# Performance work log

Hardware: AMD Instinct MI355X
Metric: run time of the kernel (lower is better)

## Reference

```python
import jax, jax.numpy as jnp
import numpy as np

B, L, C = 2, 2048, 2048
H, HKV, D = 16, 4, 128  # heads, kv heads, head_dim
G = H // HKV            # GQA group size
NEG = -1e9


def rms_norm(x, w, eps=1e-6):
    # FastRMSNorm: compute in fp32, scale by weight, cast back
    xf = x.astype(jnp.float32)
    y = xf * jax.lax.rsqrt(jnp.mean(xf * xf, axis=-1, keepdims=True) + eps) * w
    return y.astype(x.dtype)


def apply_rope(t, cos, sin):
    # t: (B, h, L, D); cos/sin: (L, D//2) broadcast to (1,1,L,D//2)
    t1, t2 = jnp.split(t, 2, axis=-1)
    c = cos[None, None]
    s = sin[None, None]
    return jnp.concatenate([t1 * c - t2 * s, t2 * c + t1 * s], axis=-1)


def setup_inputs() -> dict:
    key = jax.random.key(0)
    ks = jax.random.split(key, 8)
    x = jax.random.normal(ks[0], (B, L, C), jnp.float32)
    Wq = jax.random.normal(ks[1], (H * D, C), jnp.float32) * 0.02
    Wk = jax.random.normal(ks[2], (HKV * D, C), jnp.float32) * 0.02
    Wv = jax.random.normal(ks[3], (HKV * D, C), jnp.float32) * 0.02
    Wo = jax.random.normal(ks[4], (C, H * D), jnp.float32) * 0.02
    q_norm_w = jnp.ones((D,), jnp.float32)
    k_norm_w = jnp.ones((D,), jnp.float32)
    pos = jnp.arange(L, dtype=jnp.float32)[:, None]
    inv_freq = 1.0 / (10000.0 ** (jnp.arange(0, D, 2, dtype=jnp.float32) / D))
    ang = pos * inv_freq[None, :]            # (L, D//2)
    rope_cos = jnp.cos(ang)
    rope_sin = jnp.sin(ang)
    # VAR-style block-causal visibility: 8 blocks of 256, query block i sees key blocks <= i
    blk = jnp.arange(L) // 256
    vis = blk[None, :] <= blk[:, None]       # (L, L) bool
    attn_bias = jnp.where(vis, 0.0, NEG).astype(jnp.float32)[None, None]  # (1,1,L,L)
    return dict(x=x, Wq=Wq, Wk=Wk, Wv=Wv, Wo=Wo, q_norm_w=q_norm_w,
                k_norm_w=k_norm_w, rope_cos=rope_cos, rope_sin=rope_sin,
                attn_bias=attn_bias)


def reference(x, Wq, Wk, Wv, Wo, q_norm_w, k_norm_w, rope_cos, rope_sin, attn_bias):
    b, l, c = x.shape
    # fused projections -> (B, h, L, D)
    q = rms_norm((x @ Wq.T).reshape(b, l, H, D), q_norm_w).transpose(0, 2, 1, 3)
    k = rms_norm((x @ Wk.T).reshape(b, l, HKV, D), k_norm_w).transpose(0, 2, 1, 3)
    v = (x @ Wv.T).reshape(b, l, HKV, D).transpose(0, 2, 1, 3)
    q = apply_rope(q, rope_cos, rope_sin)
    k = apply_rope(k, rope_cos, rope_sin)
    scale = D ** -0.5
    # GQA: group query heads over kv heads
    qg = q.reshape(b, HKV, G, l, D)
    scores = jnp.einsum('bkgqd,bkKd->bkgqK', qg, k) * scale
    scores = scores + attn_bias[:, :, None]  # broadcast (1,1,1,L,L)
    probs = jax.nn.softmax(scores, axis=-1)
    out = jnp.einsum('bkgqK,bkKd->bkgqd', probs, v)
    out = out.reshape(b, H, l, D).transpose(0, 2, 1, 3).reshape(b, l, H * D)
    return out @ Wo.T
```

## Files before the change

### kernel.cpp

```cpp
#include <hip/hip_runtime.h>

#define B_ 2
#define L_ 2048
#define C_ 2048
#define H_ 16
#define HKV_ 4
#define D_ 128
#define G_ (H_ / HKV_)
#define TOK_ (B_ * L_)
#define NQKV_ 3072

typedef __bf16 bf16;
typedef __bf16 bf16x4 __attribute__((ext_vector_type(4)));
typedef __bf16 bf16x8 __attribute__((ext_vector_type(8)));
typedef float f32x4 __attribute__((ext_vector_type(4)));

__device__ inline void gload16(const void* g, void* l) {
  __builtin_amdgcn_global_load_lds(
      (const __attribute__((address_space(1))) void*)g,
      (__attribute__((address_space(3))) void*)l, 16, 0, 0);
}

__global__ void cvt_bf16(const float* __restrict__ in, bf16* __restrict__ out, int n4) {
  int stride = gridDim.x * blockDim.x;
  for (int j = blockIdx.x * blockDim.x + threadIdx.x; j < n4; j += stride) {
    float4 v = reinterpret_cast<const float4*>(in)[j];
    bf16x4 o = {(bf16)v.x, (bf16)v.y, (bf16)v.z, (bf16)v.w};
    reinterpret_cast<bf16x4*>(out)[j] = o;
  }
}

template <bool OUT_F32>
__global__ __launch_bounds__(256) void gemm_bt(
    const bf16* __restrict__ A, const bf16* __restrict__ Bm,
    void* __restrict__ Cm, int M, int N, int K) {
  __shared__ __align__(16) bf16 sA[128 * 32];
  __shared__ __align__(16) bf16 sB[128 * 32];
  const int tid = threadIdx.x;
  const int row0 = blockIdx.x * 128, col0 = blockIdx.y * 128;
  const int wid = tid >> 6, lane = tid & 63;
  const int wr = wid >> 1, wc = wid & 1;
  const int l15 = lane & 15, kk = (lane >> 4) * 8;
  f32x4 acc[4][4] = {};
  const int nk = K / 32;
  const int f0 = tid;
  const int r0 = f0 >> 2, c0 = f0 & 3;
  const int f1 = 256 + tid;
  const int r1 = f1 >> 2, c1 = f1 & 3;
  const int ldsA0 = (wid * 64) * 8, ldsA1 = (256 + wid * 64) * 8;
  for (int kt = 0; kt < nk; ++kt) {
    __syncthreads();
    gload16(A + (size_t)(row0 + r0) * K + kt * 32 + c0 * 8, sA + ldsA0);
    gload16(A + (size_t)(row0 + r1) * K + kt * 32 + c1 * 8, sA + ldsA1);
    gload16(Bm + (size_t)(col0 + r0) * K + kt * 32 + c0 * 8, sB + ldsA0);
    gload16(Bm + (size_t)(col0 + r1) * K + kt * 32 + c1 * 8, sB + ldsA1);
    __syncthreads();
    bf16x8 af[4], bfr[4];
#pragma unroll
    for (int m = 0; m < 4; ++m)
      af[m] = *reinterpret_cast<const bf16x8*>(sA + (wr * 64 + m * 16 + l15) * 32 + kk);
#pragma unroll
    for (int n = 0; n < 4; ++n)
      bfr[n] = *reinterpret_cast<const bf16x8*>(sB + (wc * 64 + n * 16 + l15) * 32 + kk);
#pragma unroll
    for (int m = 0; m < 4; ++m)
#pragma unroll
      for (int n = 0; n < 4; ++n)
        acc[m][n] = __builtin_amdgcn_mfma_f32_16x16x32_bf16(af[m], bfr[n], acc[m][n], 0, 0, 0);
  }
#pragma unroll
  for (int m = 0; m < 4; ++m)
#pragma unroll
    for (int n = 0; n < 4; ++n)
#pragma unroll
      for (int r = 0; r < 4; ++r) {
        int row = row0 + wr * 64 + m * 16 + (lane >> 4) * 4 + r;
        int col = col0 + wc * 64 + n * 16 + l15;
        if constexpr (OUT_F32)
          reinterpret_cast<float*>(Cm)[(size_t)row * N + col] = acc[m][n][r];
        else
          reinterpret_cast<bf16*>(Cm)[(size_t)row * N + col] = (bf16)acc[m][n][r];
      }
}

__global__ void k_norm_rope(const bf16* __restrict__ proj,
                            const float* __restrict__ normw,
                            const float* __restrict__ cosb,
                            const float* __restrict__ sinb,
                            bf16* __restrict__ out) {
  int wid = (blockIdx.x * blockDim.x + threadIdx.x) >> 6;
  int lane = threadIdx.x & 63;
  int head = wid & 3, tok = wid >> 2;
  int b = tok / L_, l = tok % L_;
  const bf16* p = proj + (size_t)tok * NQKV_ + H_ * D_ + head * D_;
  float t1 = (float)p[lane];
  float t2 = (float)p[lane + 64];
  float ss = t1 * t1 + t2 * t2;
#pragma unroll
  for (int off = 32; off; off >>= 1) ss += __shfl_xor(ss, off);
  float r = rsqrtf(ss * (1.0f / 128.0f) + 1e-6f);
  float n1 = t1 * r * normw[lane];
  float n2 = t2 * r * normw[lane + 64];
  float c = cosb[l * 64 + lane], s = sinb[l * 64 + lane];
  bf16* q = out + (((size_t)b * HKV_ + head) * L_ + l) * D_;
  q[lane] = (bf16)(n1 * c - n2 * s);
  q[lane + 64] = (bf16)(n2 * c + n1 * s);
}

__global__ __launch_bounds__(256) void v_transpose(const bf16* __restrict__ proj,
                                                   bf16* __restrict__ vt) {
  __shared__ __align__(16) bf16 sT[64 * 136];
  const int t = threadIdx.x;
  const int l0 = blockIdx.x * 64;
  const int bk = blockIdx.y;
  const bf16* src = proj + (size_t)((bk >> 2) * L_ + l0) * NQKV_ + (H_ + HKV_) * D_ + (bk & 3) * D_;
#pragma unroll
  for (int c = 0; c < 4; ++c) {
    int idx = c * 256 + t;
    int l = idx >> 4, dc = idx & 15;
    bf16x8 v = *reinterpret_cast<const bf16x8*>(src + (size_t)l * NQKV_ + dc * 8);
    *reinterpret_cast<bf16x8*>((char*)sT + l * 272 + ((dc ^ (l >> 3)) << 4)) = v;
  }
  __syncthreads();
  bf16* dst = vt + (size_t)bk * D_ * L_ + l0;
#pragma unroll
  for (int c = 0; c < 4; ++c) {
    int idx = c * 256 + t;
    int d = idx >> 3, lg = idx & 7;
    bf16x8 o;
#pragma unroll
    for (int j = 0; j < 8; ++j) {
      int l = lg * 8 + j;
      o[j] = *reinterpret_cast<const bf16*>((char*)sT + l * 272 + (((d >> 3) ^ lg) << 4) + (d & 7) * 2);
    }
    *reinterpret_cast<bf16x8*>(dst + (size_t)d * L_ + lg * 8) = o;
  }
}

__global__ __launch_bounds__(512, 4) void attn_fused(
    const bf16* __restrict__ QKV,
    const bf16* __restrict__ Kn,
    const bf16* __restrict__ Vt,
    const float* __restrict__ qnw,
    const float* __restrict__ cosb, const float* __restrict__ sinb,
    bf16* __restrict__ AO) {
  __shared__ __align__(16) bf16 sK[2][64 * 128];
  __shared__ __align__(16) bf16 sV[2][64 * 128];
  __shared__ __align__(16) bf16 sP[8 * 16 * 64];
  const int tid = threadIdx.x;
  const int wid = tid >> 6, lane = tid & 63;
  const int bid = blockIdx.x;
  const int bk = bid & 7;
  const int qt = 63 - (bid >> 3);
  const int b = bk >> 2;
  const int hl = wid & 3, qs = wid >> 2;
  const int h = (bk & 3) * G_ + hl;
  const int qrow0 = qt * 32 + qs * 16;
  const int l15 = lane & 15, g4 = lane >> 4, kk = g4 * 8;

  const int qrow = qrow0 + l15;
  const bf16* qsrc = QKV + (size_t)(b * L_ + qrow) * NQKV_ + h * D_;
  float t[4][8];
  float ss = 0.f;
#pragma unroll
  for (int c = 0; c < 4; ++c) {
    bf16x8 v = *reinterpret_cast<const bf16x8*>(qsrc + c * 32 + kk);
#pragma unroll
    for (int j = 0; j < 8; ++j) { t[c][j] = (float)v[j]; ss += t[c][j] * t[c][j]; }
  }

  const int kr0 = tid >> 4, kc0 = tid & 15;
  const int kr1 = 32 + kr0;
  const int vr0 = tid >> 3, vc0 = tid & 7;
  const int vr1 = 64 + vr0;
  const bf16* kb = Kn + (size_t)bk * L_ * D_;
  const bf16* vb = Vt + (size_t)bk * D_ * (size_t)L_;
  const bf16* kp0 = kb + (size_t)kr0 * D_ + ((kc0 ^ (kr0 & 7)) * 8);
  const bf16* kp1 = kb + (size_t)kr1 * D_ + ((kc0 ^ (kr1 & 7)) * 8);
  const bf16* vp0 = vb + (size_t)vr0 * L_ + ((vc0 ^ (vr0 & 7)) * 8);
  const bf16* vp1 = vb + (size_t)vr1 * L_ + ((vc0 ^ (vr1 & 7)) * 8);

  const int ntiles = ((qt >> 3) + 1) * 4;
  gload16(kp0, &sK[0][tid * 8]);
  gload16(kp1, &sK[0][(512 + tid) * 8]);
  gload16(vp0, &sV[0][tid * 8]);
  gload16(vp1, &sV[0][(512 + tid) * 8]);

  constexpr float SCL = 0.12752650038632816f;
  ss += __shfl_xor(ss, 16);
  ss += __shfl_xor(ss, 32);
  const float rr = rsqrtf(ss * (1.0f / 128.0f) + 1e-6f);
  bf16x8 qf[4];
#pragma unroll
  for (int c = 0; c < 2; ++c)
#pragma unroll
    for (int j = 0; j < 8; ++j) {
      int i = c * 32 + kk + j;
      float n1 = t[c][j] * rr * qnw[i];
      float n2 = t[c + 2][j] * rr * qnw[i + 64];
      float cs = cosb[qrow * 64 + i], sn = sinb[qrow * 64 + i];
      qf[c][j] = (bf16)((n1 * cs - n2 * sn) * SCL);
      qf[c + 2][j] = (bf16)((n2 * cs + n1 * sn) * SCL);
    }

  bf16* myP = sP + wid * 16 * 64;
  f32x4 acc[8] = {};
  float mref[4], lpart[4];
#pragma unroll
  for (int r = 0; r < 4; ++r) { mref[r] = -1e30f; lpart[r] = 0.f; }

  __syncthreads();

  auto tile_step = [&](const bf16* sKc, const bf16* sVc, bf16* sKn_, bf16* sVn_,
                       int ktNext, bool doPref) {
    if (doPref) {
      gload16(kp0 + (size_t)ktNext * 64 * D_, &sKn_[tid * 8]);
      gload16(kp1 + (size_t)ktNext * 64 * D_, &sKn_[(512 + tid) * 8]);
      gload16(vp0 + ktNext * 64, &sVn_[tid * 8]);
      gload16(vp1 + ktNext * 64, &sVn_[(512 + tid) * 8]);
    }
    const char* cK = (const char*)sKc;
    const char* cV = (const char*)sVc;
    f32x4 s[4];
#pragma unroll
    for (int n = 0; n < 4; ++n) {
      f32x4 st = {};
#pragma unroll
      for (int c = 0; c < 4; ++c) {
        int byte = (n * 16 + l15) * 256 + ((((c << 2) + g4) ^ (l15 & 7)) << 4);
        bf16x8 kf = *reinterpret_cast<const bf16x8*>(cK + byte);
        st = __builtin_amdgcn_mfma_f32_16x16x32_bf16(qf[c], kf, st, 0, 0, 0);
      }
      s[n] = st;
    }
    float pm[4];
#pragma unroll
    for (int r = 0; r < 4; ++r)
      pm[r] = fmaxf(fmaxf(s[0][r], s[1][r]), fmaxf(s[2][r], s[3][r]));
    int ok = (pm[0] <= mref[0] + 8.f) & (pm[1] <= mref[1] + 8.f) &
             (pm[2] <= mref[2] + 8.f) & (pm[3] <= mref[3] + 8.f);
    if (!__all(ok)) {
#pragma unroll
      for (int off = 1; off < 16; off <<= 1)
#pragma unroll
        for (int r = 0; r < 4; ++r) pm[r] = fmaxf(pm[r], __shfl_xor(pm[r], off));
#pragma unroll
      for (int r = 0; r < 4; ++r) {
        float mnew = fmaxf(mref[r], pm[r]);
        float resc = exp2f(mref[r] - mnew);
        mref[r] = mnew;
        lpart[r] *= resc;
#pragma unroll
        for (int f = 0; f < 8; ++f) acc[f][r] *= resc;
      }
    }
#pragma unroll
    for (int r = 0; r < 4; ++r) {
      float lp = lpart[r];
#pragma unroll
      for (int n = 0; n < 4; ++n) {
        float p = exp2f(s[n][r] - mref[r]);
        s[n][r] = p;
        lp += p;
      }
      lpart[r] = lp;
    }
#pragma unroll
    for (int n = 0; n < 4; ++n)
#pragma unroll
      for (int r = 0; r < 4; ++r) {
        int pr = (g4 << 2) + r;
        int byte = pr * 128 + (((n * 32) + (l15 * 2)) ^ ((pr & 7) << 4));
        *reinterpret_cast<bf16*>((char*)myP + byte) = (bf16)s[n][r];
      }
    bf16x8 pf0 = *reinterpret_cast<const bf16x8*>(
        (char*)myP + l15 * 128 + ((g4 ^ (l15 & 7)) << 4));
    bf16x8 pf1 = *reinterpret_cast<const bf16x8*>(
        (char*)myP + l15 * 128 + (((4 + g4) ^ (l15 & 7)) << 4));
#pragma unroll
    for (int f = 0; f < 8; ++f) {
      int d = f * 16 + l15;
      bf16x8 vf0 = *reinterpret_cast<const bf16x8*>(
          cV + d * 128 + ((g4 ^ (l15 & 7)) << 4));
      acc[f] = __builtin_amdgcn_mfma_f32_16x16x32_bf16(pf0, vf0, acc[f], 0, 0, 0);
      bf16x8 vf1 = *reinterpret_cast<const bf16x8*>(
          cV + d * 128 + (((4 + g4) ^ (l15 & 7)) << 4));
      acc[f] = __builtin_amdgcn_mfma_f32_16x16x32_bf16(pf1, vf1, acc[f], 0, 0, 0);
    }
    __syncthreads();
  };

  for (int kt = 0; kt < ntiles; kt += 2) {
    tile_step(sK[0], sV[0], sK[1], sV[1], kt + 1, true);
    tile_step(sK[1], sV[1], sK[0], sV[0], kt + 2, kt + 2 < ntiles);
  }

#pragma unroll
  for (int off = 1; off < 16; off <<= 1)
#pragma unroll
    for (int r = 0; r < 4; ++r) lpart[r] += __shfl_xor(lpart[r], off);
  float rinv[4];
#pragma unroll
  for (int r = 0; r < 4; ++r) rinv[r] = 1.f / lpart[r];
#pragma unroll
  for (int f = 0; f < 8; ++f)
#pragma unroll
    for (int r = 0; r < 4; ++r) {
      int row = qrow0 + g4 * 4 + r;
      AO[((size_t)(b * L_ + row) * H_ + h) * D_ + f * 16 + l15] =
          (bf16)(acc[f][r] * rinv[r]);
    }
}

extern "C" void kernel_launch(void* const* d_in, const int* in_sizes, int n_in,
                              void* d_out, int out_size, void* d_ws, size_t ws_size,
                              hipStream_t stream) {
  const float* x = (const float*)d_in[0];
  const float* Wq = (const float*)d_in[1];
  const float* Wk = (const float*)d_in[2];
  const float* Wv = (const float*)d_in[3];
  const float* Wo = (const float*)d_in[4];
  const float* qnw = (const float*)d_in[5];
  const float* knw = (const float*)d_in[6];
  const float* rc = (const float*)d_in[7];
  const float* rs = (const float*)d_in[8];
  float* out = (float*)d_out;

  char* ws = (char*)d_ws;
  bf16* xb = (bf16*)ws;    ws += (size_t)TOK_ * C_ * 2;
  bf16* wqb = (bf16*)ws;   ws += (size_t)(H_ * D_) * C_ * 2;
  bf16* wkb = (bf16*)ws;   ws += (size_t)(HKV_ * D_) * C_ * 2;
  bf16* wvb = (bf16*)ws;   ws += (size_t)(HKV_ * D_) * C_ * 2;
  bf16* wob = (bf16*)ws;   ws += (size_t)C_ * (H_ * D_) * 2;
  bf16* qkv = (bf16*)ws;   ws += (size_t)TOK_ * NQKV_ * 2;
  bf16* Kb = (bf16*)ws;    ws += (size_t)TOK_ * HKV_ * D_ * 2;
  bf16* Vtb = (bf16*)ws;   ws += (size_t)TOK_ * HKV_ * D_ * 2;
  bf16* AOb = xb;

  auto cvt = [&](const float* src, bf16* dst, size_t n) {
    int n4 = (int)(n / 4);
    int grid = (n4 + 255) / 256;
    if (grid > 4096) grid = 4096;
    cvt_bf16<<<grid, 256, 0, stream>>>(src, dst, n4);
  };
  cvt(x, xb, (size_t)TOK_ * C_);
  cvt(Wq, wqb, (size_t)H_ * D_ * C_);
  cvt(Wk, wkb, (size_t)HKV_ * D_ * C_);
  cvt(Wv, wvb, (size_t)HKV_ * D_ * C_);
  cvt(Wo, wob, (size_t)C_ * H_ * D_);

  gemm_bt<false><<<dim3(TOK_ / 128, NQKV_ / 128), 256, 0, stream>>>(
      xb, wqb, qkv, TOK_, NQKV_, C_);

  k_norm_rope<<<(TOK_ * HKV_) / 4, 256, 0, stream>>>(qkv, knw, rc, rs, Kb);
  v_transpose<<<dim3(L_ / 64, B_ * HKV_), 256, 0, stream>>>(qkv, Vtb);

  attn_fused<<<512, 512, 0, stream>>>(qkv, Kb, Vtb, qnw, rc, rs, AOb);

  gemm_bt<true><<<dim3(TOK_ / 128, C_ / 128), 256, 0, stream>>>(
      AOb, wob, out, TOK_, C_, H_ * D_);
}
```

Before: 236.5 us.

## Transpose MFMA operands so each lane owns one query row in attention

Swaps the A/B operands of the QK^T and PV MFMAs so the accumulator layout puts a single query row per lane. Softmax max and sum then become per-lane scalars with two cross-group shuffles instead of four-row arrays with four-step reductions. P is written to LDS as packed bf16x4 and the output is stored as bf16x4 vectors. It also adds s_setprio around the MFMA sections and changes the block-to-query-tile mapping so the first half of the grid runs in ascending tile order and the rest descending.

```diff
diff --git a/kernel.cpp b/kernel.cpp
--- a/kernel.cpp
+++ b/kernel.cpp
@@ -151,12 +151,13 @@
   const int wid = tid >> 6, lane = tid & 63;
   const int bid = blockIdx.x;
   const int bk = bid & 7;
-  const int qt = 63 - (bid >> 3);
+  const int qt = (bid < 256) ? (bid >> 3) : 63 - ((bid - 256) >> 3);
   const int b = bk >> 2;
   const int hl = wid & 3, qs = wid >> 2;
   const int h = (bk & 3) * G_ + hl;
   const int qrow0 = qt * 32 + qs * 16;
   const int l15 = lane & 15, g4 = lane >> 4, kk = g4 * 8;
+  const int swz = (l15 & 7) << 4;
 
   const int qrow = qrow0 + l15;
   const bf16* qsrc = QKV + (size_t)(b * L_ + qrow) * NQKV_ + h * D_;
@@ -203,11 +204,9 @@
       qf[c + 2][j] = (bf16)((n2 * cs + n1 * sn) * SCL);
     }
 
-  bf16* myP = sP + wid * 16 * 64;
+  char* myP = (char*)(sP + wid * 16 * 64);
   f32x4 acc[8] = {};
-  float mref[4], lpart[4];
-#pragma unroll
-  for (int r = 0; r < 4; ++r) { mref[r] = -1e30f; lpart[r] = 0.f; }
+  float mref = -1e30f, lpart = 0.f;
 
   __syncthreads();
 
@@ -222,6 +221,7 @@
     const char* cK = (const char*)sKc;
     const char* cV = (const char*)sVc;
     f32x4 s[4];
+    __builtin_amdgcn_s_setprio(1);
 #pragma unroll
     for (int n = 0; n < 4; ++n) {
       f32x4 st = {};
@@ -229,64 +229,50 @@
       for (int c = 0; c < 4; ++c) {
         int byte = (n * 16 + l15) * 256 + ((((c << 2) + g4) ^ (l15 & 7)) << 4);
         bf16x8 kf = *reinterpret_cast<const bf16x8*>(cK + byte);
-        st = __builtin_amdgcn_mfma_f32_16x16x32_bf16(qf[c], kf, st, 0, 0, 0);
+        st = __builtin_amdgcn_mfma_f32_16x16x32_bf16(kf, qf[c], st, 0, 0, 0);
       }
       s[n] = st;
     }
-    float pm[4];
-#pragma unroll
-    for (int r = 0; r < 4; ++r)
-      pm[r] = fmaxf(fmaxf(s[0][r], s[1][r]), fmaxf(s[2][r], s[3][r]));
-    int ok = (pm[0] <= mref[0] + 8.f) & (pm[1] <= mref[1] + 8.f) &
-             (pm[2] <= mref[2] + 8.f) & (pm[3] <= mref[3] + 8.f);
-    if (!__all(ok)) {
-#pragma unroll
-      for (int off = 1; off < 16; off <<= 1)
-#pragma unroll
-        for (int r = 0; r < 4; ++r) pm[r] = fmaxf(pm[r], __shfl_xor(pm[r], off));
+    __builtin_amdgcn_s_setprio(0);
+    float pm = fmaxf(fmaxf(s[0][0], s[0][1]), fmaxf(s[0][2], s[0][3]));
+#pragma unroll
+    for (int n = 1; n < 4; ++n)
+      pm = fmaxf(pm, fmaxf(fmaxf(s[n][0], s[n][1]), fmaxf(s[n][2], s[n][3])));
+    if (!__all(pm <= mref + 8.f)) {
+      pm = fmaxf(pm, __shfl_xor(pm, 16));
+      pm = fmaxf(pm, __shfl_xor(pm, 32));
+      float mnew = fmaxf(mref, pm);
+      float resc = exp2f(mref - mnew);
+      mref = mnew;
+      lpart *= resc;
+#pragma unroll
+      for (int f = 0; f < 8; ++f) acc[f] *= resc;
+    }
+#pragma unroll
+    for (int n = 0; n < 4; ++n)
 #pragma unroll
       for (int r = 0; r < 4; ++r) {
-        float mnew = fmaxf(mref[r], pm[r]);
-        float resc = exp2f(mref[r] - mnew);
-        mref[r] = mnew;
-        lpart[r] *= resc;
-#pragma unroll
-        for (int f = 0; f < 8; ++f) acc[f][r] *= resc;
+        float p = exp2f(s[n][r] - mref);
+        s[n][r] = p;
+        lpart += p;
       }
-    }
-#pragma unroll
-    for (int r = 0; r < 4; ++r) {
-      float lp = lpart[r];
-#pragma unroll
-      for (int n = 0; n < 4; ++n) {
-        float p = exp2f(s[n][r] - mref[r]);
-        s[n][r] = p;
-        lp += p;
-      }
-      lpart[r] = lp;
-    }
-#pragma unroll
-    for (int n = 0; n < 4; ++n)
-#pragma unroll
-      for (int r = 0; r < 4; ++r) {
-        int pr = (g4 << 2) + r;
-        int byte = pr * 128 + (((n * 32) + (l15 * 2)) ^ ((pr & 7) << 4));
-        *reinterpret_cast<bf16*>((char*)myP + byte) = (bf16)s[n][r];
-      }
-    bf16x8 pf0 = *reinterpret_cast<const bf16x8*>(
-        (char*)myP + l15 * 128 + ((g4 ^ (l15 & 7)) << 4));
-    bf16x8 pf1 = *reinterpret_cast<const bf16x8*>(
-        (char*)myP + l15 * 128 + (((4 + g4) ^ (l15 & 7)) << 4));
+#pragma unroll
+    for (int n = 0; n < 4; ++n) {
+      bf16x4 pw = {(bf16)s[n][0], (bf16)s[n][1], (bf16)s[n][2], (bf16)s[n][3]};
+      *reinterpret_cast<bf16x4*>(myP + l15 * 128 + (((n << 5) + (g4 << 3)) ^ swz)) = pw;
+    }
+    bf16x8 pf0 = *reinterpret_cast<const bf16x8*>(myP + l15 * 128 + ((g4 << 4) ^ swz));
+    bf16x8 pf1 = *reinterpret_cast<const bf16x8*>(myP + l15 * 128 + ((64 + (g4 << 4)) ^ swz));
+    __builtin_amdgcn_s_setprio(1);
 #pragma unroll
     for (int f = 0; f < 8; ++f) {
       int d = f * 16 + l15;
-      bf16x8 vf0 = *reinterpret_cast<const bf16x8*>(
-          cV + d * 128 + ((g4 ^ (l15 & 7)) << 4));
-      acc[f] = __builtin_amdgcn_mfma_f32_16x16x32_bf16(pf0, vf0, acc[f], 0, 0, 0);
-      bf16x8 vf1 = *reinterpret_cast<const bf16x8*>(
-          cV + d * 128 + (((4 + g4) ^ (l15 & 7)) << 4));
-      acc[f] = __builtin_amdgcn_mfma_f32_16x16x32_bf16(pf1, vf1, acc[f], 0, 0, 0);
-    }
+      bf16x8 vf0 = *reinterpret_cast<const bf16x8*>(cV + d * 128 + ((g4 ^ (l15 & 7)) << 4));
+      acc[f] = __builtin_amdgcn_mfma_f32_16x16x32_bf16(vf0, pf0, acc[f], 0, 0, 0);
+      bf16x8 vf1 = *reinterpret_cast<const bf16x8*>(cV + d * 128 + (((4 + g4) ^ (l15 & 7)) << 4));
+      acc[f] = __builtin_amdgcn_mfma_f32_16x16x32_bf16(vf1, pf1, acc[f], 0, 0, 0);
+    }
+    __builtin_amdgcn_s_setprio(0);
     __syncthreads();
   };
 
@@ -295,21 +281,16 @@
     tile_step(sK[1], sV[1], sK[0], sV[0], kt + 2, kt + 2 < ntiles);
   }
 
-#pragma unroll
-  for (int off = 1; off < 16; off <<= 1)
-#pragma unroll
-    for (int r = 0; r < 4; ++r) lpart[r] += __shfl_xor(lpart[r], off);
-  float rinv[4];
-#pragma unroll
-  for (int r = 0; r < 4; ++r) rinv[r] = 1.f / lpart[r];
-#pragma unroll
-  for (int f = 0; f < 8; ++f)
-#pragma unroll
-    for (int r = 0; r < 4; ++r) {
-      int row = qrow0 + g4 * 4 + r;
-      AO[((size_t)(b * L_ + row) * H_ + h) * D_ + f * 16 + l15] =
-          (bf16)(acc[f][r] * rinv[r]);
-    }
+  lpart += __shfl_xor(lpart, 16);
+  lpart += __shfl_xor(lpart, 32);
+  const float rinv = 1.f / lpart;
+  bf16* aop = AO + ((size_t)(b * L_ + qrow0 + l15) * H_ + h) * D_ + (g4 << 2);
+#pragma unroll
+  for (int f = 0; f < 8; ++f) {
+    bf16x4 o = {(bf16)(acc[f][0] * rinv), (bf16)(acc[f][1] * rinv),
+                (bf16)(acc[f][2] * rinv), (bf16)(acc[f][3] * rinv)};
+    *reinterpret_cast<bf16x4*>(aop + f * 16) = o;
+  }
 }
 
 extern "C" void kernel_launch(void* const* d_in, const int* in_sizes, int n_in,
```

Measured after the change: 218.5 us. 1.08x faster.
